# Optimization experiments

Hardware: AMD Instinct MI355X
Metric: run time of the kernel (lower is better)

The kernel has to match this reference:

```python
import jax, jax.numpy as jnp
import numpy as np

N_NODES = 100000
N_EDGES = 1600000
D_FEAT = 32
EPS = 1e-12  # F.normalize clamp eps


def setup_inputs() -> dict:
    key = jax.random.key(0)
    k1, k2, k3 = jax.random.split(key, 3)
    feat = jax.random.normal(k1, (N_NODES, D_FEAT), dtype=jnp.float32)
    beta = jnp.ones((1,), dtype=jnp.float32)
    src = jax.random.randint(k2, (N_EDGES,), 0, N_NODES, dtype=jnp.int32)
    dst = jax.random.randint(k3, (N_EDGES,), 0, N_NODES, dtype=jnp.int32)
    return {"feat": feat, "beta": beta, "src": src, "dst": dst}


def reference(feat, beta, src, dst):
    N = feat.shape[0]
    # L2-normalize node features (torch.nn.functional.normalize semantics)
    norm = jnp.maximum(jnp.linalg.norm(feat, axis=-1, keepdims=True), EPS)
    norm_h = feat / norm
    # per-edge cosine similarity: u_dot_v
    cos = jnp.sum(norm_h[src] * norm_h[dst], axis=-1)  # [E]
    e = beta[0] * cos
    # edge softmax over incoming edges of each dst node
    m = jax.lax.stop_gradient(jax.ops.segment_max(e, dst, num_segments=N))
    m = jnp.where(jnp.isfinite(m), m, 0.0)  # nodes with no in-edges
    p = jnp.exp(e - m[dst])
    s = jax.ops.segment_sum(p, dst, num_segments=N)
    p = p / s[dst]
    # weighted message aggregation: u_mul_e -> sum
    out = jax.ops.segment_sum(feat[src] * p[:, None], dst, num_segments=N)
    return out
```

## Files before the change

kernel.cpp:

```cpp
#include <hip/hip_runtime.h>
#include <hip/hip_bf16.h>

#define D_FEAT 32
#define BUCKET_SHIFT 7
#define BUCKET_NODES 128
#define MAX_NB 1024
#define CHUNK_E 8192
#define REC_CHUNK 4096

typedef __attribute__((ext_vector_type(8))) unsigned short u16x8;
typedef __attribute__((ext_vector_type(8))) float f32x8;

static __device__ __forceinline__ unsigned short f2bf(float x) {
    unsigned int u = __float_as_uint(x);
    u += 0x7FFFu + ((u >> 16) & 1u);
    return (unsigned short)(u >> 16);
}
static __device__ __forceinline__ float bf2f(unsigned short b) {
    return __uint_as_float((unsigned int)b << 16);
}

__global__ __launch_bounds__(256) void prep_hist_kernel(
    const float* __restrict__ feat,
    unsigned short* __restrict__ nfb,
    float* __restrict__ inv_norm,
    const int* __restrict__ dst,
    int* __restrict__ chunk_hist,
    int n_nodes, int n_edges, int nb, int nchunk) {

    __shared__ int s_h[MAX_NB];
    int bid = blockIdx.x;
    int t = threadIdx.x;

    if (bid < nchunk) {
        for (int i = t; i < MAX_NB; i += 256) s_h[i] = 0;
        __syncthreads();
        int base = bid * CHUNK_E;
        int cnt = min(CHUNK_E, n_edges - base);
        int cnt4 = cnt >> 2;
        const int4* dst4 = reinterpret_cast<const int4*>(dst + base);
        for (int k = t; k < cnt4; k += 256) {
            int4 d4 = dst4[k];
            atomicAdd(&s_h[d4.x >> BUCKET_SHIFT], 1);
            atomicAdd(&s_h[d4.y >> BUCKET_SHIFT], 1);
            atomicAdd(&s_h[d4.z >> BUCKET_SHIFT], 1);
            atomicAdd(&s_h[d4.w >> BUCKET_SHIFT], 1);
        }
        for (int k = (cnt4 << 2) + t; k < cnt; k += 256)
            atomicAdd(&s_h[dst[base + k] >> BUCKET_SHIFT], 1);
        __syncthreads();
        for (int i = t; i < nb; i += 256)
            chunk_hist[(size_t)i * nchunk + bid] = s_h[i];
    } else {
        int g = (bid - nchunk) * 256 + t;
        int node = g >> 3;
        int lane = g & 7;
        if (node >= n_nodes) return;
        float4 v = reinterpret_cast<const float4*>(feat + (size_t)node * D_FEAT)[lane];
        float ss = v.x * v.x + v.y * v.y + v.z * v.z + v.w * v.w;
        #pragma unroll
        for (int m = 4; m; m >>= 1) ss += __shfl_xor(ss, m, 8);
        if (lane == 0) inv_norm[node] = 1.0f / fmaxf(sqrtf(ss), 1e-12f);
        ushort4 b;
        b.x = f2bf(v.x); b.y = f2bf(v.y); b.z = f2bf(v.z); b.w = f2bf(v.w);
        reinterpret_cast<ushort4*>(nfb + (size_t)node * D_FEAT)[lane] = b;
    }
}

__global__ void col_prefix_kernel(int* __restrict__ chunk_hist,
                                  int* __restrict__ total, int nchunk, int nb) {
    int wid  = (blockIdx.x * blockDim.x + threadIdx.x) >> 6;
    int lane = threadIdx.x & 63;
    if (wid >= nb) return;
    int* row = chunk_hist + (size_t)wid * nchunk;
    int run = 0;
    for (int base = 0; base < nchunk; base += 64) {
        int c = base + lane;
        int v = (c < nchunk) ? row[c] : 0;
        int incl = v;
        #pragma unroll
        for (int off = 1; off < 64; off <<= 1) {
            int n = __shfl_up(incl, off, 64);
            if (lane >= off) incl += n;
        }
        if (c < nchunk) row[c] = run + (incl - v);
        run += __shfl(incl, 63, 64);
    }
    if (lane == 0) total[wid] = run;
}

__global__ __launch_bounds__(256) void base_scan_kernel(const int* __restrict__ total,
                                                        int* __restrict__ bucket_base,
                                                        int nb, int n_edges) {
    __shared__ int s_sum[256];
    int t = threadIdx.x;
    int i0 = t * 4;
    int a[4];
    int tsum = 0;
    #pragma unroll
    for (int j = 0; j < 4; ++j) {
        a[j] = (i0 + j < nb) ? total[i0 + j] : 0;
        tsum += a[j];
    }
    s_sum[t] = tsum;
    __syncthreads();
    for (int off = 1; off < 256; off <<= 1) {
        int add = (t >= off) ? s_sum[t - off] : 0;
        __syncthreads();
        s_sum[t] += add;
        __syncthreads();
    }
    int run = s_sum[t] - tsum;
    #pragma unroll
    for (int j = 0; j < 4; ++j) {
        if (i0 + j < nb) bucket_base[i0 + j] = run;
        run += a[j];
    }
    if (t == 0) bucket_base[nb] = n_edges;
}

__global__ __launch_bounds__(512) void scatter_kernel(const int* __restrict__ src,
                                                      const int* __restrict__ dst,
                                                      const int* __restrict__ chunk_hist,
                                                      const int* __restrict__ bucket_base,
                                                      int* __restrict__ recs,
                                                      int n_edges, int nb, int nchunk) {
    __shared__ int s_cur[MAX_NB];
    __shared__ int s_off[MAX_NB + 1];
    __shared__ int s_gbase[MAX_NB];
    __shared__ int s_sum[512];
    __shared__ int s_rec[CHUNK_E];
    __shared__ unsigned short s_b[CHUNK_E];

    int c = blockIdx.x;
    int t = threadIdx.x;
    int base = c * CHUNK_E;
    int cnt = min(CHUNK_E, n_edges - base);
    int cnt4 = cnt >> 2;
    const int4* dst4 = reinterpret_cast<const int4*>(dst + base);
    const int4* src4 = reinterpret_cast<const int4*>(src + base);

    for (int i = t; i < MAX_NB; i += 512) s_cur[i] = 0;
    __syncthreads();
    for (int k = t; k < cnt4; k += 512) {
        int4 d4 = dst4[k];
        atomicAdd(&s_cur[d4.x >> BUCKET_SHIFT], 1);
        atomicAdd(&s_cur[d4.y >> BUCKET_SHIFT], 1);
        atomicAdd(&s_cur[d4.z >> BUCKET_SHIFT], 1);
        atomicAdd(&s_cur[d4.w >> BUCKET_SHIFT], 1);
    }
    for (int k = (cnt4 << 2) + t; k < cnt; k += 512)
        atomicAdd(&s_cur[dst[base + k] >> BUCKET_SHIFT], 1);
    __syncthreads();

    int i0 = t * 2;
    int a0 = s_cur[i0], a1 = s_cur[i0 + 1];
    int tsum = a0 + a1;
    s_sum[t] = tsum;
    __syncthreads();
    for (int off = 1; off < 512; off <<= 1) {
        int add = (t >= off) ? s_sum[t - off] : 0;
        __syncthreads();
        s_sum[t] += add;
        __syncthreads();
    }
    int run = s_sum[t] - tsum;
    s_off[i0] = run;
    s_off[i0 + 1] = run + a0;
    if (t == 511) s_off[MAX_NB] = run + tsum;
    __syncthreads();
    for (int i = t; i < MAX_NB; i += 512) s_cur[i] = s_off[i];
    for (int i = t; i < nb; i += 512)
        s_gbase[i] = bucket_base[i] + chunk_hist[(size_t)i * nchunk + c];
    __syncthreads();

    for (int k = t; k < cnt4; k += 512) {
        int4 d4 = dst4[k];
        int4 s4 = src4[k];
        #pragma unroll
        for (int j = 0; j < 4; ++j) {
            int d = (j == 0) ? d4.x : (j == 1) ? d4.y : (j == 2) ? d4.z : d4.w;
            int s = (j == 0) ? s4.x : (j == 1) ? s4.y : (j == 2) ? s4.z : s4.w;
            int bb = d >> BUCKET_SHIFT;
            int lpos = atomicAdd(&s_cur[bb], 1);
            s_rec[lpos] = (s << BUCKET_SHIFT) | (d & (BUCKET_NODES - 1));
            s_b[lpos] = (unsigned short)bb;
        }
    }
    for (int k = (cnt4 << 2) + t; k < cnt; k += 512) {
        int d = dst[base + k];
        int s = src[base + k];
        int bb = d >> BUCKET_SHIFT;
        int lpos = atomicAdd(&s_cur[bb], 1);
        s_rec[lpos] = (s << BUCKET_SHIFT) | (d & (BUCKET_NODES - 1));
        s_b[lpos] = (unsigned short)bb;
    }
    __syncthreads();

    for (int i = t; i < cnt; i += 512) {
        int bb = s_b[i];
        recs[s_gbase[bb] + (i - s_off[bb])] = s_rec[i];
    }
}

__global__ __launch_bounds__(512) void bucket_aggregate_kernel(
    const unsigned short* __restrict__ nfb,
    const float* __restrict__ inv_norm,
    const int* __restrict__ bucket_base,
    const int* __restrict__ recs,
    const float* __restrict__ beta,
    float* __restrict__ out, int n_nodes) {

    __shared__ int s_rec[REC_CHUNK];
    __shared__ int s_hist[64];
    __shared__ int s_off[65];
    __shared__ float s_part[64][36];

    int blk = blockIdx.x;
    int b    = blk >> 1;
    int half = blk & 1;
    int node0 = b * BUCKET_NODES + half * 64;
    int start = bucket_base[b];
    int end   = bucket_base[b + 1];
    int t = threadIdx.x;
    int group = t >> 2;
    int lane  = t & 3;
    int nodeLocal = group & 63;
    int sub = group >> 6;
    float bscale = beta[0];

    int myv = node0 + nodeLocal;
    f32x8 bn;
    f32x8 acc;
    float ssum = 0.f;
    #pragma unroll
    for (int j = 0; j < 8; ++j) { bn[j] = 0.f; acc[j] = 0.f; }
    if (myv < n_nodes) {
        u16x8 braw = reinterpret_cast<const u16x8*>(nfb + (size_t)myv * D_FEAT)[lane];
        float invv = inv_norm[myv];
        #pragma unroll
        for (int j = 0; j < 8; ++j) bn[j] = bf2f(braw[j]) * invv;
    }

    for (int cbase = start; cbase < end; cbase += REC_CHUNK) {
        int cnt = min(REC_CHUNK, end - cbase);

        int r[8];
        #pragma unroll
        for (int j = 0; j < 8; ++j) {
            int k = t + j * 512;
            r[j] = (k < cnt) ? recs[cbase + k] : -1;
        }

        if (t < 64) s_hist[t] = 0;
        __syncthreads();
        #pragma unroll
        for (int j = 0; j < 8; ++j)
            if (r[j] >= 0) {
                int dl = r[j] & (BUCKET_NODES - 1);
                if ((dl >> 6) == half) atomicAdd(&s_hist[dl & 63], 1);
            }
        __syncthreads();

        if (t < 64) {
            int v = s_hist[t];
            int incl = v;
            #pragma unroll
            for (int off = 1; off < 64; off <<= 1) {
                int n = __shfl_up(incl, off, 64);
                if (t >= off) incl += n;
            }
            s_off[t + 1] = incl;
            if (t == 0) s_off[0] = 0;
            s_hist[t] = incl - v;
        }
        __syncthreads();

        #pragma unroll
        for (int j = 0; j < 8; ++j)
            if (r[j] >= 0) {
                int dl = r[j] & (BUCKET_NODES - 1);
                if ((dl >> 6) == half) {
                    int pos = atomicAdd(&s_hist[dl & 63], 1);
                    s_rec[pos] = r[j];
                }
            }
        __syncthreads();

        {
            int rs = s_off[nodeLocal];
            int re = s_off[nodeLocal + 1];
            int i = rs + sub;

            int u0 = 0; float inv0 = 0.f;
            u16x8 raw0;
            #pragma unroll
            for (int j = 0; j < 8; ++j) raw0[j] = 0;
            if (i < re) {
                u0 = ((unsigned)s_rec[i]) >> BUCKET_SHIFT;
                inv0 = inv_norm[u0];
                raw0 = reinterpret_cast<const u16x8*>(nfb + (size_t)u0 * D_FEAT)[lane];
            }
            for (; i < re; i += 2) {
                int u1 = 0; float inv1 = 0.f;
                u16x8 raw1;
                #pragma unroll
                for (int j = 0; j < 8; ++j) raw1[j] = 0;
                if (i + 2 < re) {
                    u1 = ((unsigned)s_rec[i + 2]) >> BUCKET_SHIFT;
                    inv1 = inv_norm[u1];
                    raw1 = reinterpret_cast<const u16x8*>(nfb + (size_t)u1 * D_FEAT)[lane];
                }
                f32x8 a;
                float d = 0.f;
                #pragma unroll
                for (int j = 0; j < 8; ++j) {
                    a[j] = bf2f(raw0[j]);
                    d = fmaf(a[j], bn[j], d);
                }
                d += __shfl_xor(d, 1, 4);
                d += __shfl_xor(d, 2, 4);
                float pe = __expf(bscale * d * inv0);
                #pragma unroll
                for (int j = 0; j < 8; ++j) acc[j] = fmaf(pe, a[j], acc[j]);
                ssum += pe;
                raw0 = raw1; inv0 = inv1;
            }
        }
        __syncthreads();
    }

    if (sub == 0) {
        float* p = &s_part[nodeLocal][lane * 8];
        #pragma unroll
        for (int j = 0; j < 8; ++j) p[j] = acc[j];
        if (lane == 0) s_part[nodeLocal][32] = ssum;
    }
    __syncthreads();
    if (sub == 1 && myv < n_nodes) {
        const float* p = &s_part[nodeLocal][lane * 8];
        #pragma unroll
        for (int j = 0; j < 8; ++j) acc[j] += p[j];
        ssum += s_part[nodeLocal][32];
        float inv_s = (ssum > 0.f) ? (1.0f / ssum) : 0.0f;
        float* op = out + (size_t)myv * D_FEAT + lane * 8;
        reinterpret_cast<float4*>(op)[0] =
            make_float4(acc[0] * inv_s, acc[1] * inv_s, acc[2] * inv_s, acc[3] * inv_s);
        reinterpret_cast<float4*>(op)[1] =
            make_float4(acc[4] * inv_s, acc[5] * inv_s, acc[6] * inv_s, acc[7] * inv_s);
    }
}

__global__ void prep_kernel(const float* __restrict__ feat,
                            unsigned short* __restrict__ nfb,
                            float* __restrict__ inv_norm, int n_nodes) {
    int g = blockIdx.x * blockDim.x + threadIdx.x;
    int node = g >> 3;
    int lane = g & 7;
    if (node >= n_nodes) return;
    float4 v = reinterpret_cast<const float4*>(feat + (size_t)node * D_FEAT)[lane];
    float ss = v.x * v.x + v.y * v.y + v.z * v.z + v.w * v.w;
    #pragma unroll
    for (int m = 4; m; m >>= 1) ss += __shfl_xor(ss, m, 8);
    if (lane == 0) inv_norm[node] = 1.0f / fmaxf(sqrtf(ss), 1e-12f);
    ushort4 b;
    b.x = f2bf(v.x); b.y = f2bf(v.y); b.z = f2bf(v.z); b.w = f2bf(v.w);
    reinterpret_cast<ushort4*>(nfb + (size_t)node * D_FEAT)[lane] = b;
}

__global__ void link_packed_kernel(const int* __restrict__ src,
                                   const int* __restrict__ dst,
                                   int* __restrict__ head,
                                   int2* __restrict__ rec, int n_edges) {
    int stride = gridDim.x * blockDim.x;
    for (int e = blockIdx.x * blockDim.x + threadIdx.x; e < n_edges; e += stride) {
        int d = dst[e];
        int s = src[e];
        int old = atomicExch(&head[d], e);
        rec[e] = make_int2(old, s);
    }
}

__global__ void fused_chase_bf16_kernel(const unsigned short* __restrict__ nfb,
                                        const float* __restrict__ inv_norm,
                                        const int* __restrict__ head,
                                        const int2* __restrict__ rec,
                                        const float* __restrict__ beta,
                                        float* __restrict__ out, int n_nodes) {
    int g = blockIdx.x * blockDim.x + threadIdx.x;
    int node = g >> 2;
    int lane = g & 3;
    if (node >= n_nodes) return;

    float bscale = beta[0];
    float invv = inv_norm[node];
    u16x8 braw = reinterpret_cast<const u16x8*>(nfb + (size_t)node * D_FEAT)[lane];
    f32x8 bn;
    #pragma unroll
    for (int j = 0; j < 8; ++j) bn[j] = bf2f(braw[j]) * invv;

    f32x8 acc;
    #pragma unroll
    for (int j = 0; j < 8; ++j) acc[j] = 0.f;
    float ssum = 0.f;

    int e = head[node];
    while (e >= 0) {
        int2 r = rec[e];
        int en = r.x, u = r.y;
        float invu = inv_norm[u];
        u16x8 araw = reinterpret_cast<const u16x8*>(nfb + (size_t)u * D_FEAT)[lane];
        f32x8 a;
        float d = 0.f;
        #pragma unroll
        for (int j = 0; j < 8; ++j) {
            a[j] = bf2f(araw[j]);
            d = fmaf(a[j], bn[j], d);
        }
        d += __shfl_xor(d, 1, 4);
        d += __shfl_xor(d, 2, 4);
        float pe = __expf(bscale * d * invu);
        #pragma unroll
        for (int j = 0; j < 8; ++j) acc[j] = fmaf(pe, a[j], acc[j]);
        ssum += pe;
        e = en;
    }

    float inv_s = (ssum > 0.f) ? (1.0f / ssum) : 0.0f;
    float* op = out + (size_t)node * D_FEAT + lane * 8;
    reinterpret_cast<float4*>(op)[0] =
        make_float4(acc[0] * inv_s, acc[1] * inv_s, acc[2] * inv_s, acc[3] * inv_s);
    reinterpret_cast<float4*>(op)[1] =
        make_float4(acc[4] * inv_s, acc[5] * inv_s, acc[6] * inv_s, acc[7] * inv_s);
}

__global__ void node_invnorm_kernel(const float* __restrict__ feat,
                                    float* __restrict__ inv_norm, int n_nodes) {
    int g = blockIdx.x * blockDim.x + threadIdx.x;
    int node = g >> 3;
    int lane = g & 7;
    if (node >= n_nodes) return;
    float4 v = reinterpret_cast<const float4*>(feat + (size_t)node * D_FEAT)[lane];
    float ss = v.x * v.x + v.y * v.y + v.z * v.z + v.w * v.w;
    #pragma unroll
    for (int m = 4; m; m >>= 1) ss += __shfl_xor(ss, m, 8);
    if (lane == 0) inv_norm[node] = 1.0f / fmaxf(sqrtf(ss), 1e-12f);
}

__global__ void edge_p_kernel(const float* __restrict__ feat,
                              const float* __restrict__ inv_norm,
                              const int* __restrict__ src,
                              const int* __restrict__ dst,
                              const float* __restrict__ beta,
                              float* __restrict__ p, float* __restrict__ s,
                              int n_edges) {
    int g = blockIdx.x * blockDim.x + threadIdx.x;
    int e = g >> 3;
    int lane = g & 7;
    if (e >= n_edges) return;
    int u = src[e];
    int v = dst[e];
    float4 a = reinterpret_cast<const float4*>(feat + (size_t)u * D_FEAT)[lane];
    float4 b = reinterpret_cast<const float4*>(feat + (size_t)v * D_FEAT)[lane];
    float d = a.x * b.x;
    d = fmaf(a.y, b.y, d);
    d = fmaf(a.z, b.z, d);
    d = fmaf(a.w, b.w, d);
    #pragma unroll
    for (int m = 4; m; m >>= 1) d += __shfl_xor(d, m, 8);
    if (lane == 0) {
        float pe = __expf(beta[0] * d * inv_norm[u] * inv_norm[v]);
        p[e] = pe;
        atomicAdd(&s[v], pe);
    }
}

__global__ void aggregate_atomic_kernel(const float* __restrict__ feat,
                                        const int* __restrict__ src,
                                        const int* __restrict__ dst,
                                        const float* __restrict__ p,
                                        const float* __restrict__ s,
                                        float* __restrict__ out, int n_edges) {
    int g = blockIdx.x * blockDim.x + threadIdx.x;
    int e = g >> 5;
    int lane = g & 31;
    if (e >= n_edges) return;
    int u = src[e];
    int v = dst[e];
    float w = p[e] / s[v];
    atomicAdd(&out[(size_t)v * D_FEAT + lane], feat[(size_t)u * D_FEAT + lane] * w);
}

extern "C" void kernel_launch(void* const* d_in, const int* in_sizes, int n_in,
                              void* d_out, int out_size, void* d_ws, size_t ws_size,
                              hipStream_t stream) {
    const float* feat = (const float*)d_in[0];
    const float* beta = (const float*)d_in[1];
    const int*   src  = (const int*)d_in[2];
    const int*   dst  = (const int*)d_in[3];
    float* out = (float*)d_out;

    int n_nodes = in_sizes[0] / D_FEAT;
    int n_edges = in_sizes[2];
    int nb = (n_nodes + BUCKET_NODES - 1) / BUCKET_NODES;
    int nchunk = (n_edges + CHUNK_E - 1) / CHUNK_E;

    size_t nfb_bytes = (size_t)n_nodes * D_FEAT * 2;
    size_t need_sort = nfb_bytes +
                       ((size_t)n_nodes + (nb + 1) + MAX_NB +
                        (size_t)nb * nchunk + (size_t)n_edges) * 4;
    size_t need_ll = nfb_bytes + (size_t)n_nodes * 8 + (size_t)n_edges * 8;

    bool sort_ok = (ws_size >= need_sort) && (nb <= MAX_NB) &&
                   (n_nodes <= (1 << 24));

    if (sort_ok) {
        unsigned short* nfb = (unsigned short*)d_ws;
        float* inv_norm   = (float*)((char*)d_ws + nfb_bytes);
        int* bucket_base  = (int*)(inv_norm + n_nodes);
        int* total        = bucket_base + (nb + 1);
        int* chunk_hist   = total + MAX_NB;
        int* recs         = chunk_hist + (size_t)nb * nchunk;

        {
            int prep_blocks = (n_nodes * 8 + 255) / 256;
            prep_hist_kernel<<<nchunk + prep_blocks, 256, 0, stream>>>(
                feat, nfb, inv_norm, dst, chunk_hist, n_nodes, n_edges, nb, nchunk);
        }
        {
            int blocks = (nb + 3) / 4;
            col_prefix_kernel<<<blocks, 256, 0, stream>>>(chunk_hist, total, nchunk, nb);
        }
        base_scan_kernel<<<1, 256, 0, stream>>>(total, bucket_base, nb, n_edges);
        scatter_kernel<<<nchunk, 512, 0, stream>>>(src, dst, chunk_hist, bucket_base,
                                                   recs, n_edges, nb, nchunk);
        bucket_aggregate_kernel<<<nb * 2, 512, 0, stream>>>(
            nfb, inv_norm, bucket_base, recs, beta, out, n_nodes);
    } else if (ws_size >= need_ll) {
        unsigned short* nfb = (unsigned short*)d_ws;
        float* inv_norm = (float*)((char*)d_ws + nfb_bytes);
        int*   head     = (int*)(inv_norm + n_nodes);
        int2*  rec      = (int2*)(head + n_nodes);

        hipMemsetAsync(head, 0xFF, (size_t)n_nodes * sizeof(int), stream);
        {
            int tt = n_nodes * 8;
            prep_kernel<<<(tt + 255) / 256, 256, 0, stream>>>(feat, nfb, inv_norm, n_nodes);
        }
        link_packed_kernel<<<2048, 256, 0, stream>>>(src, dst, head, rec, n_edges);
        {
            int tt = n_nodes * 4;
            fused_chase_bf16_kernel<<<(tt + 255) / 256, 256, 0, stream>>>(
                nfb, inv_norm, head, rec, beta, out, n_nodes);
        }
    } else {
        float* inv_norm = (float*)d_ws;
        float* s_sum    = inv_norm + n_nodes;
        float* p        = s_sum + n_nodes;

        hipMemsetAsync(s_sum, 0, (size_t)n_nodes * sizeof(float), stream);
        hipMemsetAsync(out, 0, (size_t)out_size * sizeof(float), stream);

        {
            int tt = n_nodes * 8;
            node_invnorm_kernel<<<(tt + 255) / 256, 256, 0, stream>>>(feat, inv_norm, n_nodes);
        }
        {
            long long tt = (long long)n_edges * 8;
            edge_p_kernel<<<(int)((tt + 255) / 256), 256, 0, stream>>>(
                feat, inv_norm, src, dst, beta, p, s_sum, n_edges);
        }
        {
            long long tt = (long long)n_edges * 32;
            aggregate_atomic_kernel<<<(int)((tt + 255) / 256), 256, 0, stream>>>(
                feat, src, dst, p, s_sum, out, n_edges);
        }
    }
}
```

Measured before the change: 65.57 us.

## Replace bucket base scan with atomic allocation and use 1024-thread aggregation blocks

Drops the single-block base_scan kernel. Each bucket's output region is now claimed with an atomicAdd on a global counter inside col_prefix, so bucket regions are no longer laid out in bucket order, and the aggregate kernel computes each bucket's end from base plus total. The aggregate kernel moves to 1024 threads, with four sub-groups per node whose partial sums are reduced in shared memory, and its gather stride goes from 2 to 4. This removes one launch and the serial scan at the cost of global atomics and heavier per-block reduction.

```diff
diff --git a/kernel.cpp b/kernel.cpp
--- a/kernel.cpp
+++ b/kernel.cpp
@@ -26,11 +26,14 @@
     float* __restrict__ inv_norm,
     const int* __restrict__ dst,
     int* __restrict__ chunk_hist,
+    int* __restrict__ alloc,
     int n_nodes, int n_edges, int nb, int nchunk) {
 
     __shared__ int s_h[MAX_NB];
     int bid = blockIdx.x;
     int t = threadIdx.x;
+
+    if (bid == 0 && t == 0) *alloc = 0;
 
     if (bid < nchunk) {
         for (int i = t; i < MAX_NB; i += 256) s_h[i] = 0;
@@ -68,7 +71,10 @@
 }
 
 __global__ void col_prefix_kernel(int* __restrict__ chunk_hist,
-                                  int* __restrict__ total, int nchunk, int nb) {
+                                  int* __restrict__ total,
+                                  int* __restrict__ bucket_base,
+                                  int* __restrict__ alloc,
+                                  int nchunk, int nb) {
     int wid  = (blockIdx.x * blockDim.x + threadIdx.x) >> 6;
     int lane = threadIdx.x & 63;
     if (wid >= nb) return;
@@ -86,37 +92,10 @@
         if (c < nchunk) row[c] = run + (incl - v);
         run += __shfl(incl, 63, 64);
     }
-    if (lane == 0) total[wid] = run;
-}
-
-__global__ __launch_bounds__(256) void base_scan_kernel(const int* __restrict__ total,
-                                                        int* __restrict__ bucket_base,
-                                                        int nb, int n_edges) {
-    __shared__ int s_sum[256];
-    int t = threadIdx.x;
-    int i0 = t * 4;
-    int a[4];
-    int tsum = 0;
-    #pragma unroll
-    for (int j = 0; j < 4; ++j) {
-        a[j] = (i0 + j < nb) ? total[i0 + j] : 0;
-        tsum += a[j];
-    }
-    s_sum[t] = tsum;
-    __syncthreads();
-    for (int off = 1; off < 256; off <<= 1) {
-        int add = (t >= off) ? s_sum[t - off] : 0;
-        __syncthreads();
-        s_sum[t] += add;
-        __syncthreads();
-    }
-    int run = s_sum[t] - tsum;
-    #pragma unroll
-    for (int j = 0; j < 4; ++j) {
-        if (i0 + j < nb) bucket_base[i0 + j] = run;
-        run += a[j];
-    }
-    if (t == 0) bucket_base[nb] = n_edges;
+    if (lane == 0) {
+        total[wid] = run;
+        bucket_base[wid] = atomicAdd(alloc, run);
+    }
 }
 
 __global__ __launch_bounds__(512) void scatter_kernel(const int* __restrict__ src,
@@ -203,10 +182,11 @@
     }
 }
 
-__global__ __launch_bounds__(512) void bucket_aggregate_kernel(
+__global__ __launch_bounds__(1024) void bucket_aggregate_kernel(
     const unsigned short* __restrict__ nfb,
     const float* __restrict__ inv_norm,
     const int* __restrict__ bucket_base,
+    const int* __restrict__ total,
     const int* __restrict__ recs,
     const float* __restrict__ beta,
     float* __restrict__ out, int n_nodes) {
@@ -214,14 +194,14 @@
     __shared__ int s_rec[REC_CHUNK];
     __shared__ int s_hist[64];
     __shared__ int s_off[65];
-    __shared__ float s_part[64][36];
+    __shared__ float s_part[3][64][36];
 
     int blk = blockIdx.x;
     int b    = blk >> 1;
     int half = blk & 1;
     int node0 = b * BUCKET_NODES + half * 64;
     int start = bucket_base[b];
-    int end   = bucket_base[b + 1];
+    int end   = start + total[b];
     int t = threadIdx.x;
     int group = t >> 2;
     int lane  = t & 3;
@@ -245,17 +225,17 @@
     for (int cbase = start; cbase < end; cbase += REC_CHUNK) {
         int cnt = min(REC_CHUNK, end - cbase);
 
-        int r[8];
-        #pragma unroll
-        for (int j = 0; j < 8; ++j) {
-            int k = t + j * 512;
+        int r[4];
+        #pragma unroll
+        for (int j = 0; j < 4; ++j) {
+            int k = t + j * 1024;
             r[j] = (k < cnt) ? recs[cbase + k] : -1;
         }
 
         if (t < 64) s_hist[t] = 0;
         __syncthreads();
         #pragma unroll
-        for (int j = 0; j < 8; ++j)
+        for (int j = 0; j < 4; ++j)
             if (r[j] >= 0) {
                 int dl = r[j] & (BUCKET_NODES - 1);
                 if ((dl >> 6) == half) atomicAdd(&s_hist[dl & 63], 1);
@@ -277,7 +257,7 @@
         __syncthreads();
 
         #pragma unroll
-        for (int j = 0; j < 8; ++j)
+        for (int j = 0; j < 4; ++j)
             if (r[j] >= 0) {
                 int dl = r[j] & (BUCKET_NODES - 1);
                 if ((dl >> 6) == half) {
@@ -301,13 +281,13 @@
                 inv0 = inv_norm[u0];
                 raw0 = reinterpret_cast<const u16x8*>(nfb + (size_t)u0 * D_FEAT)[lane];
             }
-            for (; i < re; i += 2) {
+            for (; i < re; i += 4) {
                 int u1 = 0; float inv1 = 0.f;
                 u16x8 raw1;
                 #pragma unroll
                 for (int j = 0; j < 8; ++j) raw1[j] = 0;
-                if (i + 2 < re) {
-                    u1 = ((unsigned)s_rec[i + 2]) >> BUCKET_SHIFT;
+                if (i + 4 < re) {
+                    u1 = ((unsigned)s_rec[i + 4]) >> BUCKET_SHIFT;
                     inv1 = inv_norm[u1];
                     raw1 = reinterpret_cast<const u16x8*>(nfb + (size_t)u1 * D_FEAT)[lane];
                 }
@@ -330,18 +310,21 @@
         __syncthreads();
     }
 
-    if (sub == 0) {
-        float* p = &s_part[nodeLocal][lane * 8];
+    if (sub != 0) {
+        float* p = &s_part[sub - 1][nodeLocal][lane * 8];
         #pragma unroll
         for (int j = 0; j < 8; ++j) p[j] = acc[j];
-        if (lane == 0) s_part[nodeLocal][32] = ssum;
-    }
-    __syncthreads();
-    if (sub == 1 && myv < n_nodes) {
-        const float* p = &s_part[nodeLocal][lane * 8];
-        #pragma unroll
-        for (int j = 0; j < 8; ++j) acc[j] += p[j];
-        ssum += s_part[nodeLocal][32];
+        if (lane == 0) s_part[sub - 1][nodeLocal][32] = ssum;
+    }
+    __syncthreads();
+    if (sub == 0 && myv < n_nodes) {
+        #pragma unroll
+        for (int s = 0; s < 3; ++s) {
+            const float* p = &s_part[s][nodeLocal][lane * 8];
+            #pragma unroll
+            for (int j = 0; j < 8; ++j) acc[j] += p[j];
+            ssum += s_part[s][nodeLocal][32];
+        }
         float inv_s = (ssum > 0.f) ? (1.0f / ssum) : 0.0f;
         float* op = out + (size_t)myv * D_FEAT + lane * 8;
         reinterpret_cast<float4*>(op)[0] =
@@ -518,6 +501,7 @@
         unsigned short* nfb = (unsigned short*)d_ws;
         float* inv_norm   = (float*)((char*)d_ws + nfb_bytes);
         int* bucket_base  = (int*)(inv_norm + n_nodes);
+        int* alloc        = bucket_base + nb;
         int* total        = bucket_base + (nb + 1);
         int* chunk_hist   = total + MAX_NB;
         int* recs         = chunk_hist + (size_t)nb * nchunk;
@@ -525,17 +509,18 @@
         {
             int prep_blocks = (n_nodes * 8 + 255) / 256;
             prep_hist_kernel<<<nchunk + prep_blocks, 256, 0, stream>>>(
-                feat, nfb, inv_norm, dst, chunk_hist, n_nodes, n_edges, nb, nchunk);
+                feat, nfb, inv_norm, dst, chunk_hist, alloc,
+                n_nodes, n_edges, nb, nchunk);
         }
         {
             int blocks = (nb + 3) / 4;
-            col_prefix_kernel<<<blocks, 256, 0, stream>>>(chunk_hist, total, nchunk, nb);
-        }
-        base_scan_kernel<<<1, 256, 0, stream>>>(total, bucket_base, nb, n_edges);
+            col_prefix_kernel<<<blocks, 256, 0, stream>>>(
+                chunk_hist, total, bucket_base, alloc, nchunk, nb);
+        }
         scatter_kernel<<<nchunk, 512, 0, stream>>>(src, dst, chunk_hist, bucket_base,
                                                    recs, n_edges, nb, nchunk);
-        bucket_aggregate_kernel<<<nb * 2, 512, 0, stream>>>(
-            nfb, inv_norm, bucket_base, recs, beta, out, n_nodes);
+        bucket_aggregate_kernel<<<nb * 2, 1024, 0, stream>>>(
+            nfb, inv_norm, bucket_base, total, recs, beta, out, n_nodes);
     } else if (ws_size >= need_ll) {
         unsigned short* nfb = (unsigned short*)d_ws;
         float* inv_norm = (float*)((char*)d_ws + nfb_bytes);
```

Measured after the change: 83.44 us. 1.27x slower.
